# Kernel tuning notes

Measured on AMD Instinct MI355X. Metric: run time of the kernel, lower is better.

## Reference

```python
import jax, jax.numpy as jnp
import numpy as np

D = 4                      # corr_disp / max_displacement
K = 2 * D + 1              # window side -> K*K = 81 displacement channels
C = 256                    # in_channels


def shifted_patches(x, d):
    """x: [B,C,H,W] -> [B,C,K*K,H,W]; patch k=(dy*K+dx) is x shifted by
    (dy-d, dx-d) with zero padding (matches Correlation/NaiveAssemble2 indexing)."""
    B, Ch, H, W = x.shape
    xp = jnp.pad(x, ((0, 0), (0, 0), (d, d), (d, d)))
    k = 2 * d + 1
    sl = [xp[:, :, dy:dy + H, dx:dx + W] for dy in range(k) for dx in range(k)]
    return jnp.stack(sl, axis=2)


def conv2d(x, w, b, pad):
    y = jax.lax.conv_general_dilated(
        x, w, window_strides=(1, 1), padding=[(pad, pad), (pad, pad)],
        dimension_numbers=('NCHW', 'OIHW', 'NCHW'))
    return y + b[None, :, None, None]


def setup_inputs() -> dict:
    key = jax.random.key(0)
    ks = jax.random.split(key, 12)
    B, H, W = 2, 64, 64
    std = 0.01
    return {
        'feat':     jax.random.normal(ks[0], (B, C, H, W), jnp.float32),
        'feat_ref': jax.random.normal(ks[1], (B, C, H, W), jnp.float32),
        # ConcatUpdate conv stack: 2C->256 (1x1), 256->16 (3x3), 16->3 (3x3), 3->2 (3x3)
        'w1': jax.random.normal(ks[2], (256, 2 * C, 1, 1), jnp.float32) * std,
        'b1': jnp.zeros((256,), jnp.float32),
        'w2': jax.random.normal(ks[3], (16, 256, 3, 3), jnp.float32) * std,
        'b2': jnp.zeros((16,), jnp.float32),
        'w3': jax.random.normal(ks[4], (3, 16, 3, 3), jnp.float32) * std,
        'b3': jnp.zeros((3,), jnp.float32),
        'w4': jax.random.normal(ks[5], (2, 3, 3, 3), jnp.float32) * std,
        'b4': jnp.array([1.0, 0.0], jnp.float32),  # init_weights: bias[0]=1, bias[1]=0
    }


def reference(feat, feat_ref, w1, b1, w2, b2, w3, b3, w4, b4):
    # Correlation (cost volume over (2D+1)^2 displacements, kernel_size=1)
    patches = shifted_patches(feat_ref, D)                    # [B,C,K2,H,W]
    aff = jnp.einsum('bchw,bckhw->bkhw', feat, patches)       # [B,K2,H,W]
    # sum-normalize over displacement channels (use_softmax_norm=False)
    aff = aff / (jnp.sum(aff, axis=1, keepdims=True) + 1e-7)
    # NaiveAssemble2: windowed weighted gather of feat_ref
    aligned = jnp.einsum('bkhw,bckhw->bchw', aff, patches)    # [B,C,H,W]
    # ConcatUpdate
    cat = jnp.concatenate([feat, aligned], axis=1)            # [B,2C,H,W]
    h = conv2d(cat, w1, b1, 0)
    h = conv2d(h, w2, b2, 1)
    h = conv2d(h, w3, b3, 1)
    logits = conv2d(h, w4, b4, 1)                             # [B,2,H,W]
    score = jax.nn.softmax(logits, axis=1)
    return score[:, 0:1] * feat + score[:, 1:2] * aligned
```

## Files before the change

### kernel.cpp

```cpp
#include <hip/hip_runtime.h>
#include <hip/hip_bf16.h>
#include <math.h>

#define BATCH 2
#define CCH   256
#define HH    64
#define WW    64
#define PIX   (HH*WW)
#define K2    81
#define BP_N  (BATCH*PIX)

__global__ void k_transpose(const float* __restrict__ in, float* __restrict__ out) {
    __shared__ float tile[32][33];
    int b  = blockIdx.z;
    int p0 = blockIdx.x * 32;
    int c0 = blockIdx.y * 32;
    int tx = threadIdx.x;
    int ty = threadIdx.y;
    const float* ib = in  + (size_t)b * CCH * PIX;
    float*       ob = out + (size_t)b * CCH * PIX;
    #pragma unroll
    for (int i = 0; i < 4; i++) {
        int c = c0 + ty + i * 8;
        int p = p0 + tx;
        tile[ty + i * 8][tx] = ib[(size_t)c * PIX + p];
    }
    __syncthreads();
    #pragma unroll
    for (int i = 0; i < 4; i++) {
        int p = p0 + ty + i * 8;
        int c = c0 + tx;
        ob[(size_t)p * CCH + c] = tile[tx][ty + i * 8];
    }
}

__global__ void k_corr_assemble(const float* __restrict__ featT,
                                const float* __restrict__ refT,
                                float* __restrict__ alignedT) {
    int blk = blockIdx.x;
    int bp  = ((blk & 7) << 10) | (blk >> 3);
    int b  = bp >> 12;
    int p  = bp & 4095;
    int h  = p >> 6, w = p & 63;
    int tid = threadIdx.x;

    __shared__ float s_aff[K2];
    __shared__ int   s_pix[K2];
    __shared__ __align__(16) float s_affc[88];
    __shared__ __align__(16) int   s_poff[88];
    __shared__ int   s_kc[88];
    __shared__ int   s_kc_hi[24];
    __shared__ int   s_cnt0, s_cnt1;
    __shared__ float s_den;

    if (tid < K2) {
        s_aff[tid] = 0.f;
        int dy = tid / 9, dx = tid - dy * 9;
        int y = h + dy - 4, x = w + dx - 4;
        s_pix[tid] = ((unsigned)y < 64u && (unsigned)x < 64u) ? ((y << 6) | x) : -1;
    }
    __syncthreads();

    if (tid < 128) {
        bool valid = (tid < K2) && (s_pix[tid] >= 0);
        unsigned long long m = __ballot(valid);
        int lane   = tid & 63;
        int prefix = __popcll(m & ((1ULL << lane) - 1ULL));
        if (tid < 64) {
            if (valid) s_kc[prefix] = tid;
            if (tid == 0) s_cnt0 = (int)__popcll(m);
        } else {
            if (valid) s_kc_hi[prefix] = tid;
            if (tid == 64) s_cnt1 = (int)__popcll(m);
        }
    }
    __syncthreads();
    int n0 = s_cnt0, n1 = s_cnt1;
    int nv = n0 + n1;
    if (tid < n1) s_kc[n0 + tid] = s_kc_hi[tid];
    __syncthreads();
    if (tid < nv) s_poff[tid] = s_pix[s_kc[tid]] << 10;
    __syncthreads();

    const float* rb = refT + ((size_t)b << 20);

    int hw = tid >> 5;
    int j  = tid & 31;
    const float* fb = featT + ((size_t)bp << 8) + j;
    float f[8];
    #pragma unroll
    for (int t = 0; t < 8; t++) f[t] = fb[32 * t];

    for (int ii = hw; ii < nv; ii += 8) {
        int k    = s_kc[ii];
        int poff = s_poff[ii];
        const char* rp = (const char*)rb + poff + 4 * j;
        float partial = 0.f;
        #pragma unroll
        for (int t = 0; t < 8; t++)
            partial = fmaf(f[t], *(const float*)(rp + 128 * t), partial);
        partial = __fadd_rn(partial, __shfl_xor(partial, 8));
        partial = __fadd_rn(partial, __shfl_xor(partial, 16));
        partial = __fadd_rn(partial, __shfl_xor(partial, 4));
        partial = __fadd_rn(partial, __shfl_xor(partial, 2));
        partial = __fadd_rn(partial, __shfl_xor(partial, 1));
        if (j == 0) s_aff[k] = partial;
    }
    __syncthreads();

    if (tid == 0) {
        float s = 0.f;
        for (int k = 0; k < K2; k++) s = __fadd_rn(s, s_aff[k]);
        s_den = __fadd_rn(s, 1e-7f);
    }
    __syncthreads();
    if (tid < nv) s_affc[tid] = __fdiv_rn(s_aff[s_kc[tid]], s_den);
    __syncthreads();

    const char* rbc = (const char*)rb + ((size_t)tid << 2);
    float acc = 0.f;
    int i = 0;
    for (; i + 4 <= nv; i += 4) {
        float4 af = *(const float4*)&s_affc[i];
        int4   po = *(const int4*)&s_poff[i];
        float v0 = *(const float*)(rbc + po.x);
        float v1 = *(const float*)(rbc + po.y);
        float v2 = *(const float*)(rbc + po.z);
        float v3 = *(const float*)(rbc + po.w);
        acc = fmaf(af.x, v0, acc);
        acc = fmaf(af.y, v1, acc);
        acc = fmaf(af.z, v2, acc);
        acc = fmaf(af.w, v3, acc);
    }
    for (; i < nv; i++)
        acc = fmaf(s_affc[i], *(const float*)(rbc + s_poff[i]), acc);
    alignedT[((size_t)bp << 8) + tid] = acc;
}

__global__ void k_w1t(const float* __restrict__ w1, float* __restrict__ w1t) {
    __shared__ float tile[32][33];
    int c0 = blockIdx.x * 32;
    int o0 = blockIdx.y * 32;
    int tx = threadIdx.x;
    int ty = threadIdx.y;
    #pragma unroll
    for (int i = 0; i < 4; i++)
        tile[ty + i * 8][tx] = w1[(size_t)(o0 + ty + i * 8) * 512 + c0 + tx];
    __syncthreads();
    #pragma unroll
    for (int i = 0; i < 4; i++)
        w1t[(size_t)(c0 + ty + i * 8) * 256 + o0 + tx] = tile[tx][ty + i * 8];
}

__global__ void k_conv1(const float* __restrict__ featT,
                        const float* __restrict__ alignedT,
                        const float* __restrict__ w1t,
                        const float* __restrict__ b1,
                        float* __restrict__ h1) {
    __shared__ float s_a[32][68];
    __shared__ float s_b[32][68];
    int m0  = blockIdx.x * 64;
    int n0  = blockIdx.y * 64;
    int tid = threadIdx.x;
    int tx  = tid & 15;
    int ty  = tid >> 4;

    float acc[4][4] = {{0.f}};

    for (int kc = 0; kc < 16; kc++) {
        int c0 = kc * 32;
        const float* asrc;
        int coff;
        if (c0 < 256) { asrc = featT;    coff = c0; }
        else          { asrc = alignedT; coff = c0 - 256; }

        #pragma unroll
        for (int i = tid; i < 512; i += 256) {
            int cq = i & 7, px = i >> 3;
            float4 v = *(const float4*)(asrc + ((size_t)(m0 + px) << 8) + coff + (cq << 2));
            s_a[cq * 4 + 0][px] = v.x;
            s_a[cq * 4 + 1][px] = v.y;
            s_a[cq * 4 + 2][px] = v.z;
            s_a[cq * 4 + 3][px] = v.w;
        }
        #pragma unroll
        for (int i = tid; i < 512; i += 256) {
            int oq = i & 15, cc = i >> 4;
            float4 v = *(const float4*)(w1t + (size_t)(c0 + cc) * 256 + n0 + (oq << 2));
            *(float4*)&s_b[cc][oq << 2] = v;
        }
        __syncthreads();

        #pragma unroll 8
        for (int k = 0; k < 32; k++) {
            float4 av = *(const float4*)&s_a[k][ty << 2];
            float4 bv = *(const float4*)&s_b[k][tx << 2];
            acc[0][0] = fmaf(av.x, bv.x, acc[0][0]);
            acc[0][1] = fmaf(av.x, bv.y, acc[0][1]);
            acc[0][2] = fmaf(av.x, bv.z, acc[0][2]);
            acc[0][3] = fmaf(av.x, bv.w, acc[0][3]);
            acc[1][0] = fmaf(av.y, bv.x, acc[1][0]);
            acc[1][1] = fmaf(av.y, bv.y, acc[1][1]);
            acc[1][2] = fmaf(av.y, bv.z, acc[1][2]);
            acc[1][3] = fmaf(av.y, bv.w, acc[1][3]);
            acc[2][0] = fmaf(av.z, bv.x, acc[2][0]);
            acc[2][1] = fmaf(av.z, bv.y, acc[2][1]);
            acc[2][2] = fmaf(av.z, bv.z, acc[2][2]);
            acc[2][3] = fmaf(av.z, bv.w, acc[2][3]);
            acc[3][0] = fmaf(av.w, bv.x, acc[3][0]);
            acc[3][1] = fmaf(av.w, bv.y, acc[3][1]);
            acc[3][2] = fmaf(av.w, bv.z, acc[3][2]);
            acc[3][3] = fmaf(av.w, bv.w, acc[3][3]);
        }
        __syncthreads();
    }

    float4 bias = *(const float4*)(b1 + n0 + tx * 4);
    #pragma unroll
    for (int i = 0; i < 4; i++) {
        int px = m0 + ty * 4 + i;
        float4 v;
        v.x = acc[i][0] + bias.x;
        v.y = acc[i][1] + bias.y;
        v.z = acc[i][2] + bias.z;
        v.w = acc[i][3] + bias.w;
        *(float4*)(h1 + ((size_t)px << 8) + n0 + tx * 4) = v;
    }
}

__global__ void k_w2t(const float* __restrict__ w2, float* __restrict__ w2t) {
    int i = blockIdx.x * 256 + threadIdx.x;
    if (i >= 16 * 256 * 9) return;
    int o  = i / 2304;
    int r  = i % 2304;
    int c  = r / 9;
    int kk = r % 9;
    int cg = c >> 2, ci = c & 3;
    w2t[(((kk * 64 + cg) * 16 + o) << 2) + ci] = w2[i];
}

__global__ void k_conv2(const float* __restrict__ h1,
                        const float* __restrict__ w2t,
                        const float* __restrict__ b2,
                        float* __restrict__ h2) {
    __shared__ float s_in[3][18][68];
    int blk = blockIdx.x;
    int b   = blk >> 8;
    int r   = blk & 255;
    int y   = r >> 2;
    int w0  = (r & 3) * 16;
    int tid = threadIdx.x;
    int o   = tid & 15;
    int ps  = (tid >> 4) & 7;

    const float* hb = h1 + ((size_t)b << 20);

    float4 a0 = {0.f, 0.f, 0.f, 0.f};
    float4 a1 = {0.f, 0.f, 0.f, 0.f};

    for (int chunk = 0; chunk < 4; chunk++) {
        int c0 = chunk << 6;
        for (int i = tid; i < 3 * 18 * 16; i += 256) {
            int c4 = i & 15;
            int pi = (i >> 4) % 18;
            int ri = (i >> 4) / 18;
            int yy = y + ri - 1;
            int xx = w0 + pi - 1;
            float4 v = {0.f, 0.f, 0.f, 0.f};
            if ((unsigned)yy < 64u && (unsigned)xx < 64u)
                v = *(const float4*)(hb + ((size_t)((yy << 6) | xx) << 8) + c0 + (c4 << 2));
            *(float4*)&s_in[ri][pi][c4 << 2] = v;
        }
        __syncthreads();

        #pragma unroll
        for (int kk = 0; kk < 9; kk++) {
            int ky = kk / 3, kx = kk - ky * 3;
            const float* wp = w2t + (((size_t)(kk * 64 + (c0 >> 2)) * 16 + o) << 2);
            #pragma unroll 8
            for (int c4 = 0; c4 < 16; c4++) {
                float4 wv = *(const float4*)(wp + (c4 << 6));
                float4 i0 = *(const float4*)&s_in[ky][ps + kx][c4 << 2];
                float4 i1 = *(const float4*)&s_in[ky][ps + 8 + kx][c4 << 2];
                a0.x = fmaf(wv.x, i0.x, a0.x);
                a0.y = fmaf(wv.y, i0.y, a0.y);
                a0.z = fmaf(wv.z, i0.z, a0.z);
                a0.w = fmaf(wv.w, i0.w, a0.w);
                a1.x = fmaf(wv.x, i1.x, a1.x);
                a1.y = fmaf(wv.y, i1.y, a1.y);
                a1.z = fmaf(wv.z, i1.z, a1.z);
                a1.w = fmaf(wv.w, i1.w, a1.w);
            }
        }
        __syncthreads();
    }

    size_t bp0 = ((size_t)b << 12) + (y << 6) + w0;
    h2[(bp0 + ps) * 16 + o]     = ((a0.x + a0.y) + (a0.z + a0.w)) + b2[o];
    h2[(bp0 + ps + 8) * 16 + o] = ((a1.x + a1.y) + (a1.z + a1.w)) + b2[o];
}

__global__ void k_conv3(const float* __restrict__ h2,
                        const float* __restrict__ w3,
                        const float* __restrict__ b3,
                        float* __restrict__ h3) {
    int bp = blockIdx.x * 256 + threadIdx.x;
    if (bp >= BP_N) return;
    int b = bp >> 12;
    int p = bp & 4095;
    int h = p >> 6, w = p & 63;
    const float* hb = h2 + ((size_t)b << 16);

    float a0 = 0.f, a1 = 0.f, a2 = 0.f;
    #pragma unroll
    for (int kk = 0; kk < 9; kk++) {
        int ky = kk / 3, kx = kk - ky * 3;
        int y = h + ky - 1, x = w + kx - 1;
        if ((unsigned)y >= 64u || (unsigned)x >= 64u) continue;
        const float* ip = hb + (size_t)((y << 6) | x) * 16;
        #pragma unroll
        for (int c = 0; c < 16; c++) {
            float v = ip[c];
            int wi = c * 9 + kk;
            a0 = fmaf(w3[wi],       v, a0);
            a1 = fmaf(w3[144 + wi], v, a1);
            a2 = fmaf(w3[288 + wi], v, a2);
        }
    }
    h3[(size_t)bp * 3 + 0] = a0 + b3[0];
    h3[(size_t)bp * 3 + 1] = a1 + b3[1];
    h3[(size_t)bp * 3 + 2] = a2 + b3[2];
}

__global__ void k_score(const float* __restrict__ h3,
                        const float* __restrict__ w4,
                        const float* __restrict__ b4,
                        float2* __restrict__ score) {
    int bp = blockIdx.x * 256 + threadIdx.x;
    if (bp >= BP_N) return;
    int b = bp >> 12;
    int p = bp & 4095;
    int h = p >> 6, w = p & 63;
    const float* hb = h3 + (size_t)b * PIX * 3;

    float l0 = 0.f, l1 = 0.f;
    #pragma unroll
    for (int kk = 0; kk < 9; kk++) {
        int ky = kk / 3, kx = kk - ky * 3;
        int y = h + ky - 1, x = w + kx - 1;
        if ((unsigned)y >= 64u || (unsigned)x >= 64u) continue;
        const float* ip = hb + (size_t)((y << 6) | x) * 3;
        #pragma unroll
        for (int c = 0; c < 3; c++) {
            float v = ip[c];
            int wi = c * 9 + kk;
            l0 = fmaf(w4[wi],      v, l0);
            l1 = fmaf(w4[27 + wi], v, l1);
        }
    }
    l0 += b4[0];
    l1 += b4[1];

    float m  = fmaxf(l0, l1);
    float e0 = expf(l0 - m);
    float e1 = expf(l1 - m);
    float s  = e0 + e1;
    score[bp] = make_float2(e0 / s, e1 / s);
}

__global__ void k_blend(const float* __restrict__ feat,
                        const float* __restrict__ alignedT,
                        const float2* __restrict__ score,
                        float* __restrict__ out) {
    __shared__ float tile[32][33];
    int b  = blockIdx.z;
    int p0 = blockIdx.x * 32;
    int c0 = blockIdx.y * 32;
    int tx = threadIdx.x;
    int ty = threadIdx.y;

    const float* at = alignedT + ((size_t)b << 20);
    #pragma unroll
    for (int i = 0; i < 4; i++) {
        int p = p0 + ty + i * 8;
        tile[ty + i * 8][tx] = at[((size_t)p << 8) + c0 + tx];
    }
    __syncthreads();

    int p = p0 + tx;
    float2 s = score[(b << 12) + p];
    #pragma unroll
    for (int i = 0; i < 4; i++) {
        int c = c0 + ty + i * 8;
        size_t idx = (((size_t)(b * 256 + c)) << 12) + p;
        out[idx] = __fadd_rn(__fmul_rn(s.x, feat[idx]),
                             __fmul_rn(s.y, tile[tx][ty + i * 8]));
    }
}

extern "C" void kernel_launch(void* const* d_in, const int* in_sizes, int n_in,
                              void* d_out, int out_size, void* d_ws, size_t ws_size,
                              hipStream_t stream) {
    const float* feat     = (const float*)d_in[0];
    const float* feat_ref = (const float*)d_in[1];
    const float* w1 = (const float*)d_in[2];
    const float* b1 = (const float*)d_in[3];
    const float* w2 = (const float*)d_in[4];
    const float* b2 = (const float*)d_in[5];
    const float* w3 = (const float*)d_in[6];
    const float* b3 = (const float*)d_in[7];
    const float* w4 = (const float*)d_in[8];
    const float* b4 = (const float*)d_in[9];
    float* out = (float*)d_out;

    const size_t NCP = (size_t)BATCH * CCH * PIX;
    char* wsb = (char*)d_ws;
    float*  featT    = (float*)wsb;   wsb += NCP * 4;
    float*  refT     = (float*)wsb;   wsb += NCP * 4;
    float*  alignedT = (float*)wsb;   wsb += NCP * 4;
    float*  h1       = (float*)wsb;   wsb += NCP * 4;
    float*  h2       = (float*)wsb;   wsb += (size_t)BP_N * 16 * 4;
    float*  h3       = (float*)wsb;   wsb += (size_t)BP_N * 3 * 4;
    float2* sc       = (float2*)wsb;  wsb += (size_t)BP_N * 8;
    float*  w2t      = (float*)wsb;   wsb += (size_t)16 * 256 * 9 * 4;
    float*  w1t      = (float*)wsb;   wsb += (size_t)512 * 256 * 4;

    dim3 tb(32, 8, 1);
    dim3 tg(PIX / 32, CCH / 32, BATCH);
    k_transpose<<<tg, tb, 0, stream>>>(feat, featT);
    k_transpose<<<tg, tb, 0, stream>>>(feat_ref, refT);
    k_w2t<<<144, 256, 0, stream>>>(w2, w2t);
    k_w1t<<<dim3(16, 8, 1), tb, 0, stream>>>(w1, w1t);

    k_corr_assemble<<<BP_N, 256, 0, stream>>>(featT, refT, alignedT);
    k_conv1<<<dim3(BP_N / 64, 256 / 64, 1), 256, 0, stream>>>(featT, alignedT, w1t, b1, h1);
    k_conv2<<<BP_N / 16, 256, 0, stream>>>(h1, w2t, b2, h2);
    k_conv3<<<BP_N / 256, 256, 0, stream>>>(h2, w3, b3, h3);
    k_score<<<BP_N / 256, 256, 0, stream>>>(h3, w4, b4, sc);
    k_blend<<<tg, tb, 0, stream>>>(feat, alignedT, sc, out);
}
```

Baseline: 232.2 us.

## Merge prep kernels, fuse conv3 with score, unroll correlation and gather loops

```diff
diff --git a/kernel.cpp b/kernel.cpp
--- a/kernel.cpp
+++ b/kernel.cpp
@@ -10,9 +10,15 @@
 #define K2    81
 #define BP_N  (BATCH*PIX)
 
-__global__ void k_transpose(const float* __restrict__ in, float* __restrict__ out) {
+__global__ void k_transpose2(const float* __restrict__ feat,
+                             const float* __restrict__ feat_ref,
+                             float* __restrict__ featT,
+                             float* __restrict__ refT) {
     __shared__ float tile[32][33];
-    int b  = blockIdx.z;
+    int z  = blockIdx.z;
+    int b  = z & 1;
+    const float* in  = (z >> 1) ? feat_ref : feat;
+    float*       out = (z >> 1) ? refT     : featT;
     int p0 = blockIdx.x * 32;
     int c0 = blockIdx.y * 32;
     int tx = threadIdx.x;
@@ -31,6 +37,36 @@
         int p = p0 + ty + i * 8;
         int c = c0 + tx;
         ob[(size_t)p * CCH + c] = tile[tx][ty + i * 8];
+    }
+}
+
+__global__ void k_wprep(const float* __restrict__ w1, float* __restrict__ w1t,
+                        const float* __restrict__ w2, float* __restrict__ w2t) {
+    __shared__ float tile[32][33];
+    int blk = blockIdx.x;
+    int tid = threadIdx.x;
+    if (blk < 128) {
+        int c0 = (blk & 15) * 32;
+        int o0 = (blk >> 4) * 32;
+        int tx = tid & 31;
+        int ty = tid >> 5;
+        #pragma unroll
+        for (int i = 0; i < 4; i++)
+            tile[ty + i * 8][tx] = w1[(size_t)(o0 + ty + i * 8) * 512 + c0 + tx];
+        __syncthreads();
+        #pragma unroll
+        for (int i = 0; i < 4; i++)
+            w1t[(size_t)(c0 + ty + i * 8) * 256 + o0 + tx] = tile[tx][ty + i * 8];
+    } else {
+        int i = (blk - 128) * 256 + tid;
+        if (i < 16 * 256 * 9) {
+            int o  = i / 2304;
+            int r  = i % 2304;
+            int c  = r / 9;
+            int kk = r % 9;
+            int cg = c >> 2, ci = c & 3;
+            w2t[(((kk * 64 + cg) * 16 + o) << 2) + ci] = w2[i];
+        }
     }
 }
 
@@ -45,66 +81,87 @@
     int tid = threadIdx.x;
 
     __shared__ float s_aff[K2];
-    __shared__ int   s_pix[K2];
     __shared__ __align__(16) float s_affc[88];
     __shared__ __align__(16) int   s_poff[88];
-    __shared__ int   s_kc[88];
-    __shared__ int   s_kc_hi[24];
+    __shared__ __align__(8)  int2  s_kp[88];
+    __shared__ int   s_hi_k[24];
+    __shared__ int   s_hi_o[24];
     __shared__ int   s_cnt0, s_cnt1;
     __shared__ float s_den;
 
-    if (tid < K2) {
-        s_aff[tid] = 0.f;
-        int dy = tid / 9, dx = tid - dy * 9;
-        int y = h + dy - 4, x = w + dx - 4;
-        s_pix[tid] = ((unsigned)y < 64u && (unsigned)x < 64u) ? ((y << 6) | x) : -1;
-    }
-    __syncthreads();
+    int hw = tid >> 5;
+    int j  = tid & 31;
+
+    const float* fb = featT + ((size_t)bp << 8) + j;
+    float f0 = fb[0],   f1 = fb[32],  f2 = fb[64],  f3 = fb[96];
+    float f4 = fb[128], f5 = fb[160], f6 = fb[192], f7 = fb[224];
+
+    if (tid < K2) s_aff[tid] = 0.f;
 
     if (tid < 128) {
-        bool valid = (tid < K2) && (s_pix[tid] >= 0);
+        int k  = tid;
+        int dy = k / 9, dx = k - dy * 9;
+        int y  = h + dy - 4, x = w + dx - 4;
+        bool valid = (k < K2) && ((unsigned)y < 64u) && ((unsigned)x < 64u);
+        int poff = valid ? (((y << 6) | x) << 10) : 0;
         unsigned long long m = __ballot(valid);
         int lane   = tid & 63;
         int prefix = __popcll(m & ((1ULL << lane) - 1ULL));
         if (tid < 64) {
-            if (valid) s_kc[prefix] = tid;
+            if (valid) s_kp[prefix] = make_int2(k, poff);
             if (tid == 0) s_cnt0 = (int)__popcll(m);
         } else {
-            if (valid) s_kc_hi[prefix] = tid;
+            if (valid) { s_hi_k[prefix] = k; s_hi_o[prefix] = poff; }
             if (tid == 64) s_cnt1 = (int)__popcll(m);
         }
     }
     __syncthreads();
     int n0 = s_cnt0, n1 = s_cnt1;
     int nv = n0 + n1;
-    if (tid < n1) s_kc[n0 + tid] = s_kc_hi[tid];
-    __syncthreads();
-    if (tid < nv) s_poff[tid] = s_pix[s_kc[tid]] << 10;
-    __syncthreads();
-
-    const float* rb = refT + ((size_t)b << 20);
-
-    int hw = tid >> 5;
-    int j  = tid & 31;
-    const float* fb = featT + ((size_t)bp << 8) + j;
-    float f[8];
-    #pragma unroll
-    for (int t = 0; t < 8; t++) f[t] = fb[32 * t];
-
-    for (int ii = hw; ii < nv; ii += 8) {
-        int k    = s_kc[ii];
-        int poff = s_poff[ii];
-        const char* rp = (const char*)rb + poff + 4 * j;
-        float partial = 0.f;
-        #pragma unroll
-        for (int t = 0; t < 8; t++)
-            partial = fmaf(f[t], *(const float*)(rp + 128 * t), partial);
-        partial = __fadd_rn(partial, __shfl_xor(partial, 8));
-        partial = __fadd_rn(partial, __shfl_xor(partial, 16));
-        partial = __fadd_rn(partial, __shfl_xor(partial, 4));
-        partial = __fadd_rn(partial, __shfl_xor(partial, 2));
-        partial = __fadd_rn(partial, __shfl_xor(partial, 1));
-        if (j == 0) s_aff[k] = partial;
+    if (tid < n1) s_kp[n0 + tid] = make_int2(s_hi_k[tid], s_hi_o[tid]);
+    __syncthreads();
+    if (tid < nv) s_poff[tid] = s_kp[tid].y;
+
+    const float* rb  = refT + ((size_t)b << 20);
+    const char*  rbj = (const char*)rb + 4 * j;
+
+    for (int ii = 2 * hw; ii < nv; ii += 16) {
+        int2 kp0 = s_kp[ii];
+        bool has1 = (ii + 1) < nv;
+        int2 kp1 = has1 ? s_kp[ii + 1] : kp0;
+        const char* rp0 = rbj + kp0.y;
+        const char* rp1 = rbj + kp1.y;
+        float pa = 0.f, pb = 0.f;
+        pa = fmaf(f0, *(const float*)(rp0 +   0), pa);
+        pb = fmaf(f0, *(const float*)(rp1 +   0), pb);
+        pa = fmaf(f1, *(const float*)(rp0 + 128), pa);
+        pb = fmaf(f1, *(const float*)(rp1 + 128), pb);
+        pa = fmaf(f2, *(const float*)(rp0 + 256), pa);
+        pb = fmaf(f2, *(const float*)(rp1 + 256), pb);
+        pa = fmaf(f3, *(const float*)(rp0 + 384), pa);
+        pb = fmaf(f3, *(const float*)(rp1 + 384), pb);
+        pa = fmaf(f4, *(const float*)(rp0 + 512), pa);
+        pb = fmaf(f4, *(const float*)(rp1 + 512), pb);
+        pa = fmaf(f5, *(const float*)(rp0 + 640), pa);
+        pb = fmaf(f5, *(const float*)(rp1 + 640), pb);
+        pa = fmaf(f6, *(const float*)(rp0 + 768), pa);
+        pb = fmaf(f6, *(const float*)(rp1 + 768), pb);
+        pa = fmaf(f7, *(const float*)(rp0 + 896), pa);
+        pb = fmaf(f7, *(const float*)(rp1 + 896), pb);
+        pa = __fadd_rn(pa, __shfl_xor(pa, 8));
+        pb = __fadd_rn(pb, __shfl_xor(pb, 8));
+        pa = __fadd_rn(pa, __shfl_xor(pa, 16));
+        pb = __fadd_rn(pb, __shfl_xor(pb, 16));
+        pa = __fadd_rn(pa, __shfl_xor(pa, 4));
+        pb = __fadd_rn(pb, __shfl_xor(pb, 4));
+        pa = __fadd_rn(pa, __shfl_xor(pa, 2));
+        pb = __fadd_rn(pb, __shfl_xor(pb, 2));
+        pa = __fadd_rn(pa, __shfl_xor(pa, 1));
+        pb = __fadd_rn(pb, __shfl_xor(pb, 1));
+        if (j == 0) {
+            s_aff[kp0.x] = pa;
+            if (has1) s_aff[kp1.x] = pb;
+        }
     }
     __syncthreads();
 
@@ -114,13 +171,35 @@
         s_den = __fadd_rn(s, 1e-7f);
     }
     __syncthreads();
-    if (tid < nv) s_affc[tid] = __fdiv_rn(s_aff[s_kc[tid]], s_den);
+    if (tid < nv) s_affc[tid] = __fdiv_rn(s_aff[s_kp[tid].x], s_den);
     __syncthreads();
 
     const char* rbc = (const char*)rb + ((size_t)tid << 2);
     float acc = 0.f;
     int i = 0;
-    for (; i + 4 <= nv; i += 4) {
+    for (; i + 8 <= nv; i += 8) {
+        float4 af0 = *(const float4*)&s_affc[i];
+        float4 af1 = *(const float4*)&s_affc[i + 4];
+        int4   po0 = *(const int4*)&s_poff[i];
+        int4   po1 = *(const int4*)&s_poff[i + 4];
+        float v0 = *(const float*)(rbc + po0.x);
+        float v1 = *(const float*)(rbc + po0.y);
+        float v2 = *(const float*)(rbc + po0.z);
+        float v3 = *(const float*)(rbc + po0.w);
+        float v4 = *(const float*)(rbc + po1.x);
+        float v5 = *(const float*)(rbc + po1.y);
+        float v6 = *(const float*)(rbc + po1.z);
+        float v7 = *(const float*)(rbc + po1.w);
+        acc = fmaf(af0.x, v0, acc);
+        acc = fmaf(af0.y, v1, acc);
+        acc = fmaf(af0.z, v2, acc);
+        acc = fmaf(af0.w, v3, acc);
+        acc = fmaf(af1.x, v4, acc);
+        acc = fmaf(af1.y, v5, acc);
+        acc = fmaf(af1.z, v6, acc);
+        acc = fmaf(af1.w, v7, acc);
+    }
+    if (i + 4 <= nv) {
         float4 af = *(const float4*)&s_affc[i];
         int4   po = *(const int4*)&s_poff[i];
         float v0 = *(const float*)(rbc + po.x);
@@ -131,25 +210,11 @@
         acc = fmaf(af.y, v1, acc);
         acc = fmaf(af.z, v2, acc);
         acc = fmaf(af.w, v3, acc);
+        i += 4;
     }
     for (; i < nv; i++)
         acc = fmaf(s_affc[i], *(const float*)(rbc + s_poff[i]), acc);
     alignedT[((size_t)bp << 8) + tid] = acc;
-}
-
-__global__ void k_w1t(const float* __restrict__ w1, float* __restrict__ w1t) {
-    __shared__ float tile[32][33];
-    int c0 = blockIdx.x * 32;
-    int o0 = blockIdx.y * 32;
-    int tx = threadIdx.x;
-    int ty = threadIdx.y;
-    #pragma unroll
-    for (int i = 0; i < 4; i++)
-        tile[ty + i * 8][tx] = w1[(size_t)(o0 + ty + i * 8) * 512 + c0 + tx];
-    __syncthreads();
-    #pragma unroll
-    for (int i = 0; i < 4; i++)
-        w1t[(size_t)(c0 + ty + i * 8) * 256 + o0 + tx] = tile[tx][ty + i * 8];
 }
 
 __global__ void k_conv1(const float* __restrict__ featT,
@@ -228,17 +293,6 @@
     }
 }
 
-__global__ void k_w2t(const float* __restrict__ w2, float* __restrict__ w2t) {
-    int i = blockIdx.x * 256 + threadIdx.x;
-    if (i >= 16 * 256 * 9) return;
-    int o  = i / 2304;
-    int r  = i % 2304;
-    int c  = r / 9;
-    int kk = r % 9;
-    int cg = c >> 2, ci = c & 3;
-    w2t[(((kk * 64 + cg) * 16 + o) << 2) + ci] = w2[i];
-}
-
 __global__ void k_conv2(const float* __restrict__ h1,
                         const float* __restrict__ w2t,
                         const float* __restrict__ b2,
@@ -300,59 +354,66 @@
     h2[(bp0 + ps + 8) * 16 + o] = ((a1.x + a1.y) + (a1.z + a1.w)) + b2[o];
 }
 
-__global__ void k_conv3(const float* __restrict__ h2,
-                        const float* __restrict__ w3,
-                        const float* __restrict__ b3,
-                        float* __restrict__ h3) {
-    int bp = blockIdx.x * 256 + threadIdx.x;
-    if (bp >= BP_N) return;
-    int b = bp >> 12;
-    int p = bp & 4095;
-    int h = p >> 6, w = p & 63;
+__global__ void k_conv34(const float* __restrict__ h2,
+                         const float* __restrict__ w3,
+                         const float* __restrict__ b3,
+                         const float* __restrict__ w4,
+                         const float* __restrict__ b4,
+                         float2* __restrict__ score) {
+    __shared__ float s_h2[16][20][21];
+    __shared__ float s_h3[3][18][18];
+    int x0 = blockIdx.x * 16;
+    int y0 = blockIdx.y * 16;
+    int b  = blockIdx.z;
+    int tid = threadIdx.x;
+
     const float* hb = h2 + ((size_t)b << 16);
 
-    float a0 = 0.f, a1 = 0.f, a2 = 0.f;
+    for (int i = tid; i < 20 * 20 * 16; i += 256) {
+        int c  = i & 15;
+        int pq = i >> 4;
+        int rx = pq % 20, ry = pq / 20;
+        int yy = y0 + ry - 2, xx = x0 + rx - 2;
+        float v = 0.f;
+        if ((unsigned)yy < 64u && (unsigned)xx < 64u)
+            v = hb[((size_t)((yy << 6) | xx) << 4) + c];
+        s_h2[c][ry][rx] = v;
+    }
+    __syncthreads();
+
+    for (int q = tid; q < 18 * 18; q += 256) {
+        int rx3 = q % 18, ry3 = q / 18;
+        int yy = y0 + ry3 - 1, xx = x0 + rx3 - 1;
+        float a0 = 0.f, a1 = 0.f, a2 = 0.f;
+        if ((unsigned)yy < 64u && (unsigned)xx < 64u) {
+            #pragma unroll
+            for (int kk = 0; kk < 9; kk++) {
+                int ky = kk / 3, kx = kk - ky * 3;
+                #pragma unroll
+                for (int c = 0; c < 16; c++) {
+                    float v = s_h2[c][ry3 + ky][rx3 + kx];
+                    int wi = c * 9 + kk;
+                    a0 = fmaf(w3[wi],       v, a0);
+                    a1 = fmaf(w3[144 + wi], v, a1);
+                    a2 = fmaf(w3[288 + wi], v, a2);
+                }
+            }
+            a0 += b3[0]; a1 += b3[1]; a2 += b3[2];
+        }
+        s_h3[0][ry3][rx3] = a0;
+        s_h3[1][ry3][rx3] = a1;
+        s_h3[2][ry3][rx3] = a2;
+    }
+    __syncthreads();
+
+    int tx = tid & 15, ty = tid >> 4;
+    float l0 = 0.f, l1 = 0.f;
     #pragma unroll
     for (int kk = 0; kk < 9; kk++) {
         int ky = kk / 3, kx = kk - ky * 3;
-        int y = h + ky - 1, x = w + kx - 1;
-        if ((unsigned)y >= 64u || (unsigned)x >= 64u) continue;
-        const float* ip = hb + (size_t)((y << 6) | x) * 16;
-        #pragma unroll
-        for (int c = 0; c < 16; c++) {
-            float v = ip[c];
-            int wi = c * 9 + kk;
-            a0 = fmaf(w3[wi],       v, a0);
-            a1 = fmaf(w3[144 + wi], v, a1);
-            a2 = fmaf(w3[288 + wi], v, a2);
-        }
-    }
-    h3[(size_t)bp * 3 + 0] = a0 + b3[0];
-    h3[(size_t)bp * 3 + 1] = a1 + b3[1];
-    h3[(size_t)bp * 3 + 2] = a2 + b3[2];
-}
-
-__global__ void k_score(const float* __restrict__ h3,
-                        const float* __restrict__ w4,
-                        const float* __restrict__ b4,
-                        float2* __restrict__ score) {
-    int bp = blockIdx.x * 256 + threadIdx.x;
-    if (bp >= BP_N) return;
-    int b = bp >> 12;
-    int p = bp & 4095;
-    int h = p >> 6, w = p & 63;
-    const float* hb = h3 + (size_t)b * PIX * 3;
-
-    float l0 = 0.f, l1 = 0.f;
-    #pragma unroll
-    for (int kk = 0; kk < 9; kk++) {
-        int ky = kk / 3, kx = kk - ky * 3;
-        int y = h + ky - 1, x = w + kx - 1;
-        if ((unsigned)y >= 64u || (unsigned)x >= 64u) continue;
-        const float* ip = hb + (size_t)((y << 6) | x) * 3;
         #pragma unroll
         for (int c = 0; c < 3; c++) {
-            float v = ip[c];
+            float v = s_h3[c][ty + ky][tx + kx];
             int wi = c * 9 + kk;
             l0 = fmaf(w4[wi],      v, l0);
             l1 = fmaf(w4[27 + wi], v, l1);
@@ -365,6 +426,7 @@
     float e0 = expf(l0 - m);
     float e1 = expf(l1 - m);
     float s  = e0 + e1;
+    int bp = (b << 12) | ((y0 + ty) << 6) | (x0 + tx);
     score[bp] = make_float2(e0 / s, e1 / s);
 }
 
@@ -420,22 +482,17 @@
     float*  alignedT = (float*)wsb;   wsb += NCP * 4;
     float*  h1       = (float*)wsb;   wsb += NCP * 4;
     float*  h2       = (float*)wsb;   wsb += (size_t)BP_N * 16 * 4;
-    float*  h3       = (float*)wsb;   wsb += (size_t)BP_N * 3 * 4;
     float2* sc       = (float2*)wsb;  wsb += (size_t)BP_N * 8;
     float*  w2t      = (float*)wsb;   wsb += (size_t)16 * 256 * 9 * 4;
     float*  w1t      = (float*)wsb;   wsb += (size_t)512 * 256 * 4;
 
     dim3 tb(32, 8, 1);
-    dim3 tg(PIX / 32, CCH / 32, BATCH);
-    k_transpose<<<tg, tb, 0, stream>>>(feat, featT);
-    k_transpose<<<tg, tb, 0, stream>>>(feat_ref, refT);
-    k_w2t<<<144, 256, 0, stream>>>(w2, w2t);
-    k_w1t<<<dim3(16, 8, 1), tb, 0, stream>>>(w1, w1t);
+    k_transpose2<<<dim3(PIX / 32, CCH / 32, 4), tb, 0, stream>>>(feat, feat_ref, featT, refT);
+    k_wprep<<<272, 256, 0, stream>>>(w1, w1t, w2, w2t);
 
     k_corr_assemble<<<BP_N, 256, 0, stream>>>(featT, refT, alignedT);
     k_conv1<<<dim3(BP_N / 64, 256 / 64, 1), 256, 0, stream>>>(featT, alignedT, w1t, b1, h1);
     k_conv2<<<BP_N / 16, 256, 0, stream>>>(h1, w2t, b2, h2);
-    k_conv3<<<BP_N / 256, 256, 0, stream>>>(h2, w3, b3, h3);
-    k_score<<<BP_N / 256, 256, 0, stream>>>(h3, w4, b4, sc);
-    k_blend<<<tg, tb, 0, stream>>>(feat, alignedT, sc, out);
-}
+    k_conv34<<<dim3(4, 4, BATCH), 256, 0, stream>>>(h2, w3, b3, w4, b4, sc);
+    k_blend<<<dim3(PIX / 32, CCH / 32, BATCH), tb, 0, stream>>>(feat, alignedT, sc, out);
+}
```

Measured after the change: 256.3 us. 1.1x slower.
